# Kernel tuning notes

Hardware: AMD Instinct MI355X
Metric: run time of the kernel (lower is better)

The kernel has to match this reference:

```python
import jax, jax.numpy as jnp
import numpy as np

B, NKV, NQ, D, H = 4, 2048, 1024, 1024, 16
HD = D // H


def setup_inputs() -> dict:
    key = jax.random.key(0)
    ks = jax.random.split(key, 9)
    s = 0.02
    return {
        "x": jax.random.normal(ks[0], (B, NKV, D), jnp.float32),
        "y": jax.random.normal(ks[1], (B, NQ, D), jnp.float32),
        "mask": jax.random.randint(ks[2], (B, NQ, NKV), 0, 2, jnp.int32),
        "W_kv": jax.random.normal(ks[3], (D, 2 * D), jnp.float32) * s,
        "b_kv": jnp.zeros((2 * D,), jnp.float32),
        "W_q": jax.random.normal(ks[4], (D, D), jnp.float32) * s,
        "b_q": jnp.zeros((D,), jnp.float32),
        "W_o": jax.random.normal(ks[5], (D, D), jnp.float32) * s,
        "b_o": jnp.zeros((D,), jnp.float32),
    }


def reference(x, y, mask, W_kv, b_kv, W_q, b_q, W_o, b_o):
    b, nkv, _ = x.shape
    nq = y.shape[1]
    kv = x @ W_kv + b_kv                                  # [B, NKV, 2D]
    q = y @ W_q + b_q                                     # [B, NQ, D]
    kv = kv.reshape(b, nkv, H, 2 * HD).transpose(0, 2, 1, 3)  # [B,H,NKV,2HD]
    q = q.reshape(b, nq, H, HD).transpose(0, 2, 1, 3)         # [B,H,NQ,HD]
    k, v = kv[..., :HD], kv[..., HD:]
    scores = jnp.einsum('bhqd,bhkd->bhqk', q, k) / jnp.sqrt(jnp.float32(HD))
    scores = jnp.where(mask[:, None, :, :] == 0, jnp.float32(-1e20), scores)
    attn = jax.nn.softmax(scores, axis=-1)
    vals = jnp.einsum('bhqk,bhkd->bhqd', attn, v)          # [B,H,NQ,HD]
    vals = vals.transpose(0, 2, 1, 3).reshape(b, nq, D)
    return vals @ W_o + b_o
```

## Files before the change

kernel.cpp:

```cpp
#include <hip/hip_runtime.h>
#include <hip/hip_bf16.h>
#include <math.h>

#define B_   4
#define NKV_ 2048
#define NQ_  1024
#define D_   1024
#define H_   16
#define HD_  64

typedef __attribute__((ext_vector_type(8))) short bf16x8;
typedef __attribute__((ext_vector_type(4))) float f32x4;

#define MFMA16x32(a, b, c) __builtin_amdgcn_mfma_f32_16x16x32_bf16((a), (b), (c), 0, 0, 0)

#define SC_LOG2 0.1803368801111244f

__device__ __forceinline__ short f2bf(float f) {
    unsigned u = __builtin_bit_cast(unsigned, f);
    u = (u + 0x7fff + ((u >> 16) & 1)) >> 16;
    return (short)u;
}
__device__ __forceinline__ unsigned cvt_pk_bf16(float lo, float hi) {
    unsigned r;
    asm("v_cvt_pk_bf16_f32 %0, %1, %2" : "=v"(r) : "v"(lo), "v"(hi));
    return r;
}
__device__ __forceinline__ void gload_lds16(const void* g, void* l) {
    __builtin_amdgcn_global_load_lds(
        (const __attribute__((address_space(1))) void*)g,
        (__attribute__((address_space(3))) void*)l, 16, 0, 0);
}
__device__ __forceinline__ void barrier_raw() {
    asm volatile("" ::: "memory");
    __builtin_amdgcn_s_barrier();
    asm volatile("" ::: "memory");
}

__global__ __launch_bounds__(256)
void prep(const float* __restrict__ Wkv, short* __restrict__ Tkv,
          const float* __restrict__ Wq,  short* __restrict__ Tq,
          const float* __restrict__ Wo,  short* __restrict__ To,
          const int* __restrict__ mask,  unsigned short* __restrict__ m16,
          const float* __restrict__ x,   short* __restrict__ xh, int n4x,
          const float* __restrict__ y,   short* __restrict__ yh, int n4y)
{
    const int bid = (int)blockIdx.x;
    if (bid < 4096) {
        const float* W; short* T; int K, N, bx, by;
        if (bid < 2048)      { W = Wkv; T = Tkv; K = D_; N = 2 * D_; bx = bid & 63;          by = bid >> 6; }
        else if (bid < 3072) { W = Wq;  T = Tq;  K = D_; N = D_;     bx = (bid - 2048) & 31; by = (bid - 2048) >> 5; }
        else                 { W = Wo;  T = To;  K = D_; N = D_;     bx = (bid - 3072) & 31; by = (bid - 3072) >> 5; }
        __shared__ float tile[32][33];
        const int tx = threadIdx.x & 31, ty = threadIdx.x >> 5;
        const int n0 = bx * 32, k0 = by * 32;
#pragma unroll
        for (int i = 0; i < 4; ++i)
            tile[ty + 8 * i][tx] = W[(size_t)(k0 + ty + 8 * i) * N + n0 + tx];
        __syncthreads();
#pragma unroll
        for (int i = 0; i < 4; ++i)
            T[(size_t)(n0 + ty + 8 * i) * K + k0 + tx] = f2bf(tile[tx][ty + 8 * i]);
    } else if (bid < 4608) {
        const int w = (bid - 4096) * 256 + threadIdx.x;
        const int4* pp = reinterpret_cast<const int4*>(mask + (size_t)w * 64);
        unsigned wg0 = 0, wg1 = 0, wg2 = 0, wg3 = 0;
#pragma unroll
        for (int i = 0; i < 16; ++i) {
            const int4 v = pp[i];
            const unsigned nib = (unsigned)(v.x != 0) | ((unsigned)(v.y != 0) << 1)
                               | ((unsigned)(v.z != 0) << 2) | ((unsigned)(v.w != 0) << 3);
            const unsigned sh = 4u * (unsigned)(i >> 2);
            if ((i & 3) == 0) wg0 |= nib << sh;
            else if ((i & 3) == 1) wg1 |= nib << sh;
            else if ((i & 3) == 2) wg2 |= nib << sh;
            else wg3 |= nib << sh;
        }
        ushort4 o;
        o.x = (unsigned short)wg0; o.y = (unsigned short)wg1;
        o.z = (unsigned short)wg2; o.w = (unsigned short)wg3;
        reinterpret_cast<ushort4*>(m16)[w] = o;
    } else {
        const int ntot = n4x + n4y;
        for (int i = (bid - 4608) * 256 + threadIdx.x; i < ntot; i += 2048 * 256) {
            const float4 v = (i < n4x)
                ? reinterpret_cast<const float4*>(x)[i]
                : reinterpret_cast<const float4*>(y)[i - n4x];
            short4 h;
            h.x = f2bf(v.x); h.y = f2bf(v.y); h.z = f2bf(v.z); h.w = f2bf(v.w);
            if (i < n4x) reinterpret_cast<short4*>(xh)[i] = h;
            else         reinterpret_cast<short4*>(yh)[i - n4x] = h;
        }
    }
}

__global__ __launch_bounds__(512, 2)
void proj256(const short* __restrict__ A, const short* __restrict__ Bm,
             const float* __restrict__ bias, short* __restrict__ Kout,
             short* __restrict__ Vtout)
{
    constexpr int K  = 1024;
    constexpr int NT = K / 32;
    constexpr int M  = B_ * NKV_;
    constexpr int N  = 2 * D_;

    __shared__ short At[4][8192];
    __shared__ short Bt[4][8192];

    const int t    = threadIdx.x;
    const int wave = t >> 6;
    const int lane = t & 63;
    const int fr   = lane & 15;
    const int kq   = lane >> 4;
    const int wm0  = (wave >> 2) * 128;
    const int wn0  = (wave & 3) * 64;

    const int gx  = N >> 8;
    const int gy  = M >> 8;
    const int lgx = __builtin_ctz(gx);
    const int bid = (int)blockIdx.x;
    const int xcd = bid & 7;
    const int j   = bid >> 3;
    const int m0  = (xcd * (gy >> 3) + (j >> lgx)) * 256;
    const int n0  = (j & (gx - 1)) * 256;

    const int r1 = t >> 2;
    const int g1 = (t & 3) ^ ((r1 >> 1) & 3);
    const int r2 = r1 + 128;

    f32x4 acc[8][4];
#pragma unroll
    for (int i = 0; i < 8; ++i)
#pragma unroll
        for (int j2 = 0; j2 < 4; ++j2) acc[i][j2] = f32x4{0.f, 0.f, 0.f, 0.f};

    auto stage = [&](int sb, int it) {
        const int kk = it << 5;
        gload_lds16(A  + (size_t)(m0 + r1) * K + kk + 8 * g1, &At[sb][wave * 512]);
        gload_lds16(A  + (size_t)(m0 + r2) * K + kk + 8 * g1, &At[sb][4096 + wave * 512]);
        gload_lds16(Bm + (size_t)(n0 + r1) * K + kk + 8 * g1, &Bt[sb][wave * 512]);
        gload_lds16(Bm + (size_t)(n0 + r2) * K + kk + 8 * g1, &Bt[sb][4096 + wave * 512]);
    };

    stage(0, 0);
    stage(1, 1);
    stage(2, 2);

    const int gsw = ((kq ^ ((fr >> 1) & 3)) << 3);
    for (int it = 0; it < NT; ++it) {
        if (it < NT - 2)       asm volatile("s_waitcnt vmcnt(8)" ::: "memory");
        else if (it == NT - 2) asm volatile("s_waitcnt vmcnt(4)" ::: "memory");
        else                   asm volatile("s_waitcnt vmcnt(0)" ::: "memory");
        barrier_raw();

        const int cb = it & 3;
        bf16x8 af[8], bf[4];
#pragma unroll
        for (int i = 0; i < 8; ++i)
            af[i] = *reinterpret_cast<const bf16x8*>(
                &At[cb][(wm0 + i * 16 + fr) * 32 + gsw]);
#pragma unroll
        for (int i = 0; i < 4; ++i)
            bf[i] = *reinterpret_cast<const bf16x8*>(
                &Bt[cb][(wn0 + i * 16 + fr) * 32 + gsw]);

        if (it + 3 < NT) stage((it + 3) & 3, it + 3);

        __builtin_amdgcn_s_setprio(1);
#pragma unroll
        for (int i = 0; i < 8; ++i)
#pragma unroll
            for (int j2 = 0; j2 < 4; ++j2)
                acc[i][j2] = MFMA16x32(af[i], bf[j2], acc[i][j2]);
        __builtin_amdgcn_s_setprio(0);
    }

#pragma unroll
    for (int i = 0; i < 8; ++i) {
#pragma unroll
        for (int j2 = 0; j2 < 4; ++j2) {
#pragma unroll
            for (int r = 0; r < 4; ++r) {
                const int m = m0 + wm0 + i * 16 + (lane >> 4) * 4 + r;
                const int n = n0 + wn0 + j2 * 16 + fr;
                const float v = acc[i][j2][r] + bias[n];
                const int b  = m >> 11;
                const int nk = m & 2047;
                const int h  = n >> 7;
                const int c  = n & 127;
                const int bh = b * H_ + h;
                if (c < 64)
                    Kout[(((size_t)bh * NKV_ + nk) << 6) + c] = f2bf(v);
                else
                    Vtout[((size_t)bh * 64 + (c - 64)) * NKV_ + nk] = f2bf(v);
            }
        }
    }
}

template<int MODE>
__global__ __launch_bounds__(256)
void gemm64(const short* __restrict__ Ahi, const short* __restrict__ Bhi,
            const float* __restrict__ bias, void* __restrict__ outv)
{
    __shared__ short At[3][2048];
    __shared__ short Bt[3][4096];

    const int M = B_ * NQ_, N = D_, K = D_;
    const int t    = threadIdx.x;
    const int wave = t >> 6;
    const int lane = t & 63;
    const int fr   = lane & 15;
    const int kq   = lane >> 4;

    const int gx  = N >> 7;
    const int gy  = M >> 6;
    const int lgx = __builtin_ctz(gx);
    const int bid = (int)blockIdx.x;
    const int xcd = bid & 7;
    const int j   = bid >> 3;
    const int m0  = (xcd * (gy >> 3) + (j >> lgx)) * 64;
    const int n0  = (j & (gx - 1)) * 128;

    const int wm0 = (wave & 1) * 32;
    const int wn0 = (wave >> 1) * 64;
    const int NT  = K >> 5;

    const int rA = t >> 2, gA = (t & 3) ^ ((rA >> 1) & 3);
    const int r1 = t >> 2,         g1 = (t & 3) ^ ((r1 >> 1) & 3);
    const int r2 = (t + 256) >> 2, g2 = (t & 3) ^ ((r2 >> 1) & 3);

    f32x4 acc[2][4];
#pragma unroll
    for (int i = 0; i < 2; ++i)
#pragma unroll
        for (int j2 = 0; j2 < 4; ++j2) acc[i][j2] = f32x4{0.f, 0.f, 0.f, 0.f};

    auto stage = [&](int sb, int it) {
        const int kk = it << 5;
        gload_lds16(Ahi + (size_t)(m0 + rA) * K + kk + 8 * gA, &At[sb][wave * 512]);
        gload_lds16(Bhi + (size_t)(n0 + r1) * K + kk + 8 * g1, &Bt[sb][wave * 512]);
        gload_lds16(Bhi + (size_t)(n0 + r2) * K + kk + 8 * g2, &Bt[sb][2048 + wave * 512]);
    };

    stage(0, 0);
    if (NT > 1) stage(1, 1);

    const int gsw = ((kq ^ ((fr >> 1) & 3)) << 3);
    for (int it = 0; it < NT; ++it) {
        if (it + 1 < NT) asm volatile("s_waitcnt vmcnt(3)" ::: "memory");
        else             asm volatile("s_waitcnt vmcnt(0)" ::: "memory");
        barrier_raw();

        const int cb = it % 3;
        bf16x8 af[2], bf[4];
#pragma unroll
        for (int i = 0; i < 2; ++i)
            af[i] = *reinterpret_cast<const bf16x8*>(&At[cb][(wm0 + i * 16 + fr) * 32 + gsw]);
#pragma unroll
        for (int i = 0; i < 4; ++i)
            bf[i] = *reinterpret_cast<const bf16x8*>(&Bt[cb][(wn0 + i * 16 + fr) * 32 + gsw]);
        if (it + 2 < NT) stage((it + 2) % 3, it + 2);

        __builtin_amdgcn_s_setprio(1);
#pragma unroll
        for (int i = 0; i < 2; ++i)
#pragma unroll
            for (int j2 = 0; j2 < 4; ++j2)
                acc[i][j2] = MFMA16x32(af[i], bf[j2], acc[i][j2]);
        __builtin_amdgcn_s_setprio(0);
    }

#pragma unroll
    for (int i = 0; i < 2; ++i)
#pragma unroll
        for (int j2 = 0; j2 < 4; ++j2)
#pragma unroll
            for (int r = 0; r < 4; ++r) {
                const int m = m0 + wm0 + i * 16 + (lane >> 4) * 4 + r;
                const int n = n0 + wn0 + j2 * 16 + fr;
                const float v = acc[i][j2][r] + bias[n];
                if (MODE == 1) {
                    short* Q_ = (short*)outv;
                    const int b = m >> 10;
                    const int q = m & 1023;
                    const int h = n >> 6;
                    const int d = n & 63;
                    Q_[(((size_t)(b * H_ + h) * NQ_ + q) << 6) + d] =
                        f2bf(v * SC_LOG2);
                } else {
                    ((float*)outv)[(size_t)m * N + n] = v;
                }
            }
}

__global__ __launch_bounds__(512)
void attn_mfma(const short* __restrict__ Q, const short* __restrict__ K,
               const short* __restrict__ Vt,
               const unsigned short* __restrict__ m16,
               float* __restrict__ Opart, float* __restrict__ Lpart)
{
    __shared__ short KtL[2][4096];
    __shared__ short VtL[2][4096];
    __shared__ short PsL[8192];

    const int t    = threadIdx.x;
    const int wave = t >> 6;
    const int lane = t & 63;
    const int fr   = lane & 15;
    const int g    = lane >> 4;

    const int bid  = (int)blockIdx.x;
    const int xcd  = bid & 7;
    const int j    = bid >> 3;
    const int bh   = xcd * 8 + (j >> 4);
    const int rest = j & 15;
    const int half = rest & 1;
    const int b    = bh >> 4;
    const int h    = bh & 15;
    const int wq0  = (rest >> 1) * 128 + wave * 16;

    const int kts = half * 16;
    const int kte = kts + 16;

    const short* Kg  = K  + (size_t)bh * NKV_ * 64;
    const short* Vtg = Vt + (size_t)bh * 64 * NKV_;

    bf16x8 qf0, qf1;
    {
        const short* Qg = Q + ((size_t)bh * NQ_ + wq0 + fr) * 64 + g * 8;
        qf0 = *reinterpret_cast<const bf16x8*>(Qg);
        qf1 = *reinterpret_cast<const bf16x8*>(Qg + 32);
    }

    bf16x8 ones;
#pragma unroll
    for (int i = 0; i < 8; ++i) ones[i] = (short)0x3F80;

    f32x4 acc_o[4];
#pragma unroll
    for (int n = 0; n < 4; ++n) acc_o[n] = f32x4{0.f, 0.f, 0.f, 0.f};
    f32x4 lacc = f32x4{0.f, 0.f, 0.f, 0.f};

    const unsigned short* mbp =
        m16 + ((size_t)b * NQ_ + wq0 + fr) * (NKV_ / 64) * 4 + g;

    const int r8   = lane >> 3;
    const int csw  = ((lane & 7) << 3) ^ (r8 << 3);
    const int swzf = (fr & 7) << 3;
    short* PsW = PsL + wave * (16 * 64);

    auto stage = [&](int nb, int kt0) {
        const short* sK = Kg + (size_t)(kt0 + wave * 8 + r8) * 64 + csw;
        gload_lds16(sK, &KtL[nb][(wave * 8) * 64]);
        const short* sV = Vtg + (size_t)(wave * 8 + r8) * NKV_ + kt0 + csw;
        gload_lds16(sV, &VtL[nb][(wave * 8) * 64]);
    };

    stage(0, kts * 64);
    asm volatile("s_waitcnt vmcnt(0)" ::: "memory");
    __syncthreads();

    const int kcol0 = (8 * g) ^ swzf;
    const int kcol1 = (32 + 8 * g) ^ swzf;

    int cur = 0;
    for (int kt = kts; kt < kte; ++kt) {
        if (kt + 1 < kte) stage(cur ^ 1, (kt + 1) * 64);

        const unsigned mskv = mbp[(size_t)kt * 4];

        const short* KB = &KtL[cur][fr * 64];
        f32x4 s_acc[4];
        __builtin_amdgcn_s_setprio(1);
#pragma unroll
        for (int t4 = 0; t4 < 4; ++t4) {
            s_acc[t4] = f32x4{0.f, 0.f, 0.f, 0.f};
            const bf16x8 kf0 = *reinterpret_cast<const bf16x8*>(KB + t4 * 1024 + kcol0);
            const bf16x8 kf1 = *reinterpret_cast<const bf16x8*>(KB + t4 * 1024 + kcol1);
            s_acc[t4] = MFMA16x32(kf0, qf0, s_acc[t4]);
            s_acc[t4] = MFMA16x32(kf1, qf1, s_acc[t4]);
        }
        __builtin_amdgcn_s_setprio(0);

        float p[16];
#pragma unroll
        for (int t4 = 0; t4 < 4; ++t4)
#pragma unroll
            for (int r = 0; r < 4; ++r) {
                const int i = 4 * t4 + r;
                const float e = __builtin_amdgcn_exp2f(s_acc[t4][r]);
                p[i] = ((mskv >> i) & 1u) ? e : 0.f;
            }

#pragma unroll
        for (int t4 = 0; t4 < 4; ++t4) {
            uint2 w;
            w.x = cvt_pk_bf16(p[4 * t4 + 0], p[4 * t4 + 1]);
            w.y = cvt_pk_bf16(p[4 * t4 + 2], p[4 * t4 + 3]);
            *reinterpret_cast<uint2*>(&PsW[fr * 64 + ((16 * t4 + 4 * g) ^ swzf)]) = w;
        }

        {
            const bf16x8 pf0 = *reinterpret_cast<const bf16x8*>(&PsW[fr * 64 + kcol0]);
            const bf16x8 pf1 = *reinterpret_cast<const bf16x8*>(&PsW[fr * 64 + kcol1]);
            const short* VB = &VtL[cur][fr * 64];
            __builtin_amdgcn_s_setprio(1);
            lacc = MFMA16x32(ones, pf0, lacc);
            lacc = MFMA16x32(ones, pf1, lacc);
#pragma unroll
            for (int n = 0; n < 4; ++n) {
                const bf16x8 vf0 = *reinterpret_cast<const bf16x8*>(VB + n * 1024 + kcol0);
                const bf16x8 vf1 = *reinterpret_cast<const bf16x8*>(VB + n * 1024 + kcol1);
                acc_o[n] = MFMA16x32(vf0, pf0, acc_o[n]);
                acc_o[n] = MFMA16x32(vf1, pf1, acc_o[n]);
            }
            __builtin_amdgcn_s_setprio(0);
        }

        asm volatile("s_waitcnt vmcnt(0)" ::: "memory");
        __syncthreads();
        cur ^= 1;
    }

    float* Op = Opart + (size_t)half * (B_ * NQ_ * D_);
    const size_t obase = ((size_t)b * NQ_ + wq0 + fr) * D_ + h * 64;
#pragma unroll
    for (int n = 0; n < 4; ++n) {
        float4 v;
        v.x = acc_o[n][0]; v.y = acc_o[n][1];
        v.z = acc_o[n][2]; v.w = acc_o[n][3];
        *reinterpret_cast<float4*>(&Op[obase + 16 * n + 4 * g]) = v;
    }
    if (g == 0)
        Lpart[(size_t)half * (B_ * H_ * NQ_) + (size_t)bh * NQ_ + wq0 + fr] = lacc[0];
}

__global__ __launch_bounds__(256)
void combine(const float* __restrict__ Opart, const float* __restrict__ Lpart,
             short* __restrict__ valshi)
{
    const size_t npart = (size_t)B_ * NQ_ * D_;
    const int n4 = (int)(npart / 4);
    for (int i = blockIdx.x * 256 + threadIdx.x; i < n4; i += 2048 * 256) {
        const int row  = i >> 8;
        const int h    = (i & 255) >> 4;
        const int b    = row >> 10;
        const int q    = row & 1023;
        const float4 o0 = reinterpret_cast<const float4*>(Opart)[i];
        const float4 o1 = reinterpret_cast<const float4*>(Opart + npart)[i];
        const size_t li = (size_t)(b * H_ + h) * NQ_ + q;
        const float inv = 1.f / (Lpart[li] + Lpart[(size_t)B_ * H_ * NQ_ + li]);
        short4 hh;
        hh.x = f2bf((o0.x + o1.x) * inv);
        hh.y = f2bf((o0.y + o1.y) * inv);
        hh.z = f2bf((o0.z + o1.z) * inv);
        hh.w = f2bf((o0.w + o1.w) * inv);
        reinterpret_cast<short4*>(valshi)[i] = hh;
    }
}

extern "C" void kernel_launch(void* const* d_in, const int* in_sizes, int n_in,
                              void* d_out, int out_size, void* d_ws, size_t ws_size,
                              hipStream_t stream)
{
    const float* x    = (const float*)d_in[0];
    const float* y    = (const float*)d_in[1];
    const int*   mask = (const int*)  d_in[2];
    const float* W_kv = (const float*)d_in[3];
    const float* b_kv = (const float*)d_in[4];
    const float* W_q  = (const float*)d_in[5];
    const float* b_q  = (const float*)d_in[6];
    const float* W_o  = (const float*)d_in[7];
    const float* b_o  = (const float*)d_in[8];
    float* out = (float*)d_out;

    char* p = (char*)d_ws;
    auto take = [&](size_t bytes) { char* r = p; p += bytes; return r; };
    short* xhi    = (short*)take((size_t)B_ * NKV_ * D_ * 2);
    short* yhi    = (short*)take((size_t)B_ * NQ_ * D_ * 2);
    short* Wkvthi = (short*)take((size_t)2 * D_ * D_ * 2);
    short* Wqthi  = (short*)take((size_t)D_ * D_ * 2);
    short* Wothi  = (short*)take((size_t)D_ * D_ * 2);
    short* Kbf    = (short*)take((size_t)B_ * H_ * NKV_ * HD_ * 2);
    short* Vtbf   = (short*)take((size_t)B_ * H_ * HD_ * NKV_ * 2);
    short* Qbf    = (short*)take((size_t)B_ * H_ * NQ_ * HD_ * 2);
    unsigned short* m16 =
        (unsigned short*)take((size_t)B_ * NQ_ * (NKV_ / 64) * 4 * 2);
    float* Opart  = (float*)take((size_t)2 * B_ * NQ_ * D_ * 4);
    float* Lpart  = (float*)take((size_t)2 * B_ * H_ * NQ_ * 4);
    short* valshi = xhi;

    prep<<<6656, 256, 0, stream>>>(W_kv, Wkvthi, W_q, Wqthi, W_o, Wothi,
                                   mask, m16,
                                   x, xhi, B_ * NKV_ * D_ / 4,
                                   y, yhi, B_ * NQ_ * D_ / 4);

    proj256<<<256, 512, 0, stream>>>(xhi, Wkvthi, b_kv, Kbf, Vtbf);

    gemm64<1><<<512, 256, 0, stream>>>(yhi, Wqthi, b_q, Qbf);

    attn_mfma<<<1024, 512, 0, stream>>>(Qbf, Kbf, Vtbf, m16, Opart, Lpart);

    combine<<<2048, 256, 0, stream>>>(Opart, Lpart, valshi);

    gemm64<2><<<512, 256, 0, stream>>>(valshi, Wothi, b_o, out);

    (void)in_sizes; (void)n_in; (void)out_size; (void)ws_size;
}
```

Baseline: 174.6 us.

## Process two 16-row query tiles per wave to reuse K/V LDS loads

Each wave now handles 32 query rows (two 16-row subtiles) instead of 16, so every K and V fragment read from LDS and every staged K/V tile feeds twice as many MFMAs. The grid is halved to 512 blocks, the P scratch buffer is doubled, and launch bounds gain a minimum-blocks hint. This aims to cut global K/V staging traffic and LDS reads per unit of work, at the cost of more registers, more LDS per block, and fewer blocks to fill the GPU.

```diff
diff --git a/kernel.cpp b/kernel.cpp
--- a/kernel.cpp
+++ b/kernel.cpp
@@ -294,7 +294,7 @@
             }
 }
 
-__global__ __launch_bounds__(512)
+__global__ __launch_bounds__(512, 4)
 void attn_mfma(const short* __restrict__ Q, const short* __restrict__ K,
                const short* __restrict__ Vt,
                const unsigned short* __restrict__ m16,
@@ -302,7 +302,7 @@
 {
     __shared__ short KtL[2][4096];
     __shared__ short VtL[2][4096];
-    __shared__ short PsL[8192];
+    __shared__ short PsL[16384];
 
     const int t    = threadIdx.x;
     const int wave = t >> 6;
@@ -313,12 +313,13 @@
     const int bid  = (int)blockIdx.x;
     const int xcd  = bid & 7;
     const int j    = bid >> 3;
-    const int bh   = xcd * 8 + (j >> 4);
-    const int rest = j & 15;
+    const int bh   = xcd * 8 + (j >> 3);
+    const int rest = j & 7;
+    const int qt   = rest >> 1;
     const int half = rest & 1;
     const int b    = bh >> 4;
     const int h    = bh & 15;
-    const int wq0  = (rest >> 1) * 128 + wave * 16;
+    const int wq0  = qt * 256 + wave * 32;
 
     const int kts = half * 16;
     const int kte = kts + 16;
@@ -326,29 +327,36 @@
     const short* Kg  = K  + (size_t)bh * NKV_ * 64;
     const short* Vtg = Vt + (size_t)bh * 64 * NKV_;
 
-    bf16x8 qf0, qf1;
+    bf16x8 qfA0, qfA1, qfB0, qfB1;
     {
         const short* Qg = Q + ((size_t)bh * NQ_ + wq0 + fr) * 64 + g * 8;
-        qf0 = *reinterpret_cast<const bf16x8*>(Qg);
-        qf1 = *reinterpret_cast<const bf16x8*>(Qg + 32);
+        qfA0 = *reinterpret_cast<const bf16x8*>(Qg);
+        qfA1 = *reinterpret_cast<const bf16x8*>(Qg + 32);
+        qfB0 = *reinterpret_cast<const bf16x8*>(Qg + 16 * 64);
+        qfB1 = *reinterpret_cast<const bf16x8*>(Qg + 16 * 64 + 32);
     }
 
     bf16x8 ones;
 #pragma unroll
     for (int i = 0; i < 8; ++i) ones[i] = (short)0x3F80;
 
-    f32x4 acc_o[4];
-#pragma unroll
-    for (int n = 0; n < 4; ++n) acc_o[n] = f32x4{0.f, 0.f, 0.f, 0.f};
-    f32x4 lacc = f32x4{0.f, 0.f, 0.f, 0.f};
-
-    const unsigned short* mbp =
+    f32x4 accA[4], accB[4];
+#pragma unroll
+    for (int n = 0; n < 4; ++n) {
+        accA[n] = f32x4{0.f, 0.f, 0.f, 0.f};
+        accB[n] = f32x4{0.f, 0.f, 0.f, 0.f};
+    }
+    f32x4 laccA = f32x4{0.f, 0.f, 0.f, 0.f};
+    f32x4 laccB = f32x4{0.f, 0.f, 0.f, 0.f};
+
+    const unsigned short* mbpA =
         m16 + ((size_t)b * NQ_ + wq0 + fr) * (NKV_ / 64) * 4 + g;
+    const unsigned short* mbpB = mbpA + (size_t)16 * (NKV_ / 64) * 4;
 
     const int r8   = lane >> 3;
     const int csw  = ((lane & 7) << 3) ^ (r8 << 3);
     const int swzf = (fr & 7) << 3;
-    short* PsW = PsL + wave * (16 * 64);
+    short* PsW = PsL + wave * (32 * 64);
 
     auto stage = [&](int nb, int kt0) {
         const short* sK = Kg + (size_t)(kt0 + wave * 8 + r8) * 64 + csw;
@@ -368,52 +376,75 @@
     for (int kt = kts; kt < kte; ++kt) {
         if (kt + 1 < kte) stage(cur ^ 1, (kt + 1) * 64);
 
-        const unsigned mskv = mbp[(size_t)kt * 4];
+        const unsigned mA = mbpA[(size_t)kt * 4];
+        const unsigned mB = mbpB[(size_t)kt * 4];
 
         const short* KB = &KtL[cur][fr * 64];
-        f32x4 s_acc[4];
+        f32x4 sA[4], sB[4];
         __builtin_amdgcn_s_setprio(1);
 #pragma unroll
         for (int t4 = 0; t4 < 4; ++t4) {
-            s_acc[t4] = f32x4{0.f, 0.f, 0.f, 0.f};
             const bf16x8 kf0 = *reinterpret_cast<const bf16x8*>(KB + t4 * 1024 + kcol0);
             const bf16x8 kf1 = *reinterpret_cast<const bf16x8*>(KB + t4 * 1024 + kcol1);
-            s_acc[t4] = MFMA16x32(kf0, qf0, s_acc[t4]);
-            s_acc[t4] = MFMA16x32(kf1, qf1, s_acc[t4]);
+            sA[t4] = f32x4{0.f, 0.f, 0.f, 0.f};
+            sA[t4] = MFMA16x32(kf0, qfA0, sA[t4]);
+            sA[t4] = MFMA16x32(kf1, qfA1, sA[t4]);
+            sB[t4] = f32x4{0.f, 0.f, 0.f, 0.f};
+            sB[t4] = MFMA16x32(kf0, qfB0, sB[t4]);
+            sB[t4] = MFMA16x32(kf1, qfB1, sB[t4]);
         }
         __builtin_amdgcn_s_setprio(0);
 
-        float p[16];
-#pragma unroll
-        for (int t4 = 0; t4 < 4; ++t4)
-#pragma unroll
-            for (int r = 0; r < 4; ++r) {
-                const int i = 4 * t4 + r;
-                const float e = __builtin_amdgcn_exp2f(s_acc[t4][r]);
-                p[i] = ((mskv >> i) & 1u) ? e : 0.f;
-            }
-
 #pragma unroll
         for (int t4 = 0; t4 < 4; ++t4) {
+            float e0 = __builtin_amdgcn_exp2f(sA[t4][0]);
+            float e1 = __builtin_amdgcn_exp2f(sA[t4][1]);
+            float e2 = __builtin_amdgcn_exp2f(sA[t4][2]);
+            float e3 = __builtin_amdgcn_exp2f(sA[t4][3]);
+            e0 = ((mA >> (4 * t4 + 0)) & 1u) ? e0 : 0.f;
+            e1 = ((mA >> (4 * t4 + 1)) & 1u) ? e1 : 0.f;
+            e2 = ((mA >> (4 * t4 + 2)) & 1u) ? e2 : 0.f;
+            e3 = ((mA >> (4 * t4 + 3)) & 1u) ? e3 : 0.f;
             uint2 w;
-            w.x = cvt_pk_bf16(p[4 * t4 + 0], p[4 * t4 + 1]);
-            w.y = cvt_pk_bf16(p[4 * t4 + 2], p[4 * t4 + 3]);
+            w.x = cvt_pk_bf16(e0, e1);
+            w.y = cvt_pk_bf16(e2, e3);
             *reinterpret_cast<uint2*>(&PsW[fr * 64 + ((16 * t4 + 4 * g) ^ swzf)]) = w;
         }
+#pragma unroll
+        for (int t4 = 0; t4 < 4; ++t4) {
+            float e0 = __builtin_amdgcn_exp2f(sB[t4][0]);
+            float e1 = __builtin_amdgcn_exp2f(sB[t4][1]);
+            float e2 = __builtin_amdgcn_exp2f(sB[t4][2]);
+            float e3 = __builtin_amdgcn_exp2f(sB[t4][3]);
+            e0 = ((mB >> (4 * t4 + 0)) & 1u) ? e0 : 0.f;
+            e1 = ((mB >> (4 * t4 + 1)) & 1u) ? e1 : 0.f;
+            e2 = ((mB >> (4 * t4 + 2)) & 1u) ? e2 : 0.f;
+            e3 = ((mB >> (4 * t4 + 3)) & 1u) ? e3 : 0.f;
+            uint2 w;
+            w.x = cvt_pk_bf16(e0, e1);
+            w.y = cvt_pk_bf16(e2, e3);
+            *reinterpret_cast<uint2*>(&PsW[(16 + fr) * 64 + ((16 * t4 + 4 * g) ^ swzf)]) = w;
+        }
 
         {
-            const bf16x8 pf0 = *reinterpret_cast<const bf16x8*>(&PsW[fr * 64 + kcol0]);
-            const bf16x8 pf1 = *reinterpret_cast<const bf16x8*>(&PsW[fr * 64 + kcol1]);
+            const bf16x8 pfA0 = *reinterpret_cast<const bf16x8*>(&PsW[fr * 64 + kcol0]);
+            const bf16x8 pfA1 = *reinterpret_cast<const bf16x8*>(&PsW[fr * 64 + kcol1]);
+            const bf16x8 pfB0 = *reinterpret_cast<const bf16x8*>(&PsW[(16 + fr) * 64 + kcol0]);
+            const bf16x8 pfB1 = *reinterpret_cast<const bf16x8*>(&PsW[(16 + fr) * 64 + kcol1]);
             const short* VB = &VtL[cur][fr * 64];
             __builtin_amdgcn_s_setprio(1);
-            lacc = MFMA16x32(ones, pf0, lacc);
-            lacc = MFMA16x32(ones, pf1, lacc);
+            laccA = MFMA16x32(ones, pfA0, laccA);
+            laccA = MFMA16x32(ones, pfA1, laccA);
+            laccB = MFMA16x32(ones, pfB0, laccB);
+            laccB = MFMA16x32(ones, pfB1, laccB);
 #pragma unroll
             for (int n = 0; n < 4; ++n) {
                 const bf16x8 vf0 = *reinterpret_cast<const bf16x8*>(VB + n * 1024 + kcol0);
                 const bf16x8 vf1 = *reinterpret_cast<const bf16x8*>(VB + n * 1024 + kcol1);
-                acc_o[n] = MFMA16x32(vf0, pf0, acc_o[n]);
-                acc_o[n] = MFMA16x32(vf1, pf1, acc_o[n]);
+                accA[n] = MFMA16x32(vf0, pfA0, accA[n]);
+                accA[n] = MFMA16x32(vf1, pfA1, accA[n]);
+                accB[n] = MFMA16x32(vf0, pfB0, accB[n]);
+                accB[n] = MFMA16x32(vf1, pfB1, accB[n]);
             }
             __builtin_amdgcn_s_setprio(0);
         }
@@ -424,16 +455,21 @@
     }
 
     float* Op = Opart + (size_t)half * (B_ * NQ_ * D_);
-    const size_t obase = ((size_t)b * NQ_ + wq0 + fr) * D_ + h * 64;
+    const size_t obA = ((size_t)b * NQ_ + wq0 + fr) * D_ + h * 64;
+    const size_t obB = obA + (size_t)16 * D_;
 #pragma unroll
     for (int n = 0; n < 4; ++n) {
-        float4 v;
-        v.x = acc_o[n][0]; v.y = acc_o[n][1];
-        v.z = acc_o[n][2]; v.w = acc_o[n][3];
-        *reinterpret_cast<float4*>(&Op[obase + 16 * n + 4 * g]) = v;
-    }
-    if (g == 0)
-        Lpart[(size_t)half * (B_ * H_ * NQ_) + (size_t)bh * NQ_ + wq0 + fr] = lacc[0];
+        float4 vA, vB;
+        vA.x = accA[n][0]; vA.y = accA[n][1]; vA.z = accA[n][2]; vA.w = accA[n][3];
+        vB.x = accB[n][0]; vB.y = accB[n][1]; vB.z = accB[n][2]; vB.w = accB[n][3];
+        *reinterpret_cast<float4*>(&Op[obA + 16 * n + 4 * g]) = vA;
+        *reinterpret_cast<float4*>(&Op[obB + 16 * n + 4 * g]) = vB;
+    }
+    if (g == 0) {
+        const size_t lbase = (size_t)half * (B_ * H_ * NQ_) + (size_t)bh * NQ_;
+        Lpart[lbase + wq0 + fr]      = laccA[0];
+        Lpart[lbase + wq0 + 16 + fr] = laccB[0];
+    }
 }
 
 __global__ __launch_bounds__(256)
@@ -500,7 +536,7 @@
 
     gemm64<1><<<512, 256, 0, stream>>>(yhi, Wqthi, b_q, Qbf);
 
-    attn_mfma<<<1024, 512, 0, stream>>>(Qbf, Kbf, Vtbf, m16, Opart, Lpart);
+    attn_mfma<<<512, 512, 0, stream>>>(Qbf, Kbf, Vtbf, m16, Opart, Lpart);
 
     combine<<<2048, 256, 0, stream>>>(Opart, Lpart, valshi);
 
```

Result: no change. 174.9 us (+0.2%).
